# Kernel tuning notes

Hardware: AMD Instinct MI355X
Metric: run time of the kernel (lower is better)

## Reference

```python
import jax, jax.numpy as jnp
import numpy as np

NUM_TOKENS = 4096
HIDDEN = 2048
INTER = 1408
NUM_EXPERTS = 8
TOP_K = 2


def setup_inputs() -> dict:
    key = jax.random.key(0)
    k1, k2, k3, k4, k5 = jax.random.split(key, 5)
    hidden_states = jax.random.normal(k1, (NUM_TOKENS, HIDDEN), dtype=jnp.float32)
    # w1: (E, 2*I, H) gate+up fused; w2: (E, H, I)
    w1 = jax.random.normal(k2, (NUM_EXPERTS, 2 * INTER, HIDDEN), dtype=jnp.float32) * (1.0 / np.sqrt(HIDDEN))
    w2 = jax.random.normal(k3, (NUM_EXPERTS, HIDDEN, INTER), dtype=jnp.float32) * (1.0 / np.sqrt(INTER))
    raw = jax.random.uniform(k4, (NUM_TOKENS, TOP_K), dtype=jnp.float32)
    topk_weights = raw / jnp.sum(raw, axis=-1, keepdims=True)  # router softmax-normalized weights
    topk_ids = jax.random.randint(k5, (NUM_TOKENS, TOP_K), 0, NUM_EXPERTS, dtype=jnp.int32)
    return {"hidden_states": hidden_states, "w1": w1, "w2": w2,
            "topk_weights": topk_weights, "topk_ids": topk_ids}


def reference(hidden_states, w1, w2, topk_weights, topk_ids):
    """Math-equivalent of fused_experts (dispatch -> grouped gate_up GEMM ->
    SwiGLU -> grouped down GEMM -> weighted scatter-combine).

    Expressed densely per expert (E is small and fixed), which yields the
    identical output to the sorted/grouped-GEMM formulation.
    """
    E = w1.shape[0]
    inter = w1.shape[1] // 2
    dtype = hidden_states.dtype
    # gate_up projection for every expert: [E, N, 2I]
    gate_up = jnp.einsum('nh,eih->eni', hidden_states, w1)
    gate, up = gate_up[..., :inter], gate_up[..., inter:]
    act = jax.nn.silu(gate) * up  # npu_swiglu: silu(first half) * second half
    # down projection: [E, N, H]
    expert_out = jnp.einsum('eni,ehi->enh', act, w2)
    # combine weight per (token, expert): sum of topk_weights where routed
    one_hot = jax.nn.one_hot(topk_ids, E, dtype=dtype)          # [N, K, E]
    combine = jnp.sum(topk_weights[:, :, None] * one_hot, axis=1)  # [N, E]
    return jnp.einsum('ne,enh->nh', combine, expert_out)
```

## Files before the change

### kernel.cpp

```cpp
#include <hip/hip_runtime.h>
#include <hip/hip_bf16.h>

#define NTOK 4096
#define HID 2048
#define INTER 1408
#define NEXP 8
#define NPAIR 8192
#define NK1 64
#define NKT2 22
#define G1SZ 24576
#define SZ2 16384

typedef short bf16x8 __attribute__((ext_vector_type(8)));
typedef float f32x4 __attribute__((ext_vector_type(4)));

__device__ __forceinline__ unsigned short f2bf(float f) {
  unsigned u = __builtin_bit_cast(unsigned, f);
  u += 0x7fffu + ((u >> 16) & 1u);
  return (unsigned short)(u >> 16);
}
__device__ __forceinline__ float bf2f(unsigned short v) {
  return __builtin_bit_cast(float, (unsigned)v << 16);
}

__device__ __forceinline__ void gload16(const void* g, void* l) {
  __builtin_amdgcn_global_load_lds(
      (const __attribute__((address_space(1))) void*)g,
      (__attribute__((address_space(3))) void*)l, 16, 0, 0);
}

__device__ __forceinline__ int xcd_swz(int lin, int nwg) {
  int xcd = lin & 7, base = lin >> 3;
  int q = nwg >> 3, r = nwg & 7;
  return (xcd < r ? xcd * (q + 1) : r * (q + 1) + (xcd - r) * q) + base;
}

#define BAR __builtin_amdgcn_s_barrier()
#define SCHED0 __builtin_amdgcn_sched_barrier(0)
#define LGKM0 asm volatile("s_waitcnt lgkmcnt(0)" ::: "memory")
#define VM4 asm volatile("s_waitcnt vmcnt(4)" ::: "memory")
#define VM3 asm volatile("s_waitcnt vmcnt(3)" ::: "memory")
#define VM0 asm volatile("s_waitcnt vmcnt(0)" ::: "memory")
#define PRIO1 __builtin_amdgcn_s_setprio(1)
#define PRIO0 __builtin_amdgcn_s_setprio(0)

__global__ void k_prep(const float* __restrict__ hs, const float* __restrict__ w1,
                       unsigned short* __restrict__ dst,
                       const int* __restrict__ ids, int* __restrict__ ctrl,
                       unsigned short* __restrict__ row_token,
                       unsigned short* __restrict__ inv_row) {
  if (blockIdx.x == 0) {
    __shared__ int cnt[NEXP], cur[NEXP];
    int t = threadIdx.x;
    if (t < NEXP) cnt[t] = 0;
    __syncthreads();
    for (int p = t; p < NPAIR; p += 512) atomicAdd(&cnt[ids[p]], 1);
    __syncthreads();
    if (t == 0) {
      int acc = 0, T = 0;
      for (int e = 0; e < NEXP; ++e) {
        cur[e] = acc;
        ctrl[e] = cnt[e];
        ctrl[8 + e] = acc;
        int n = (cnt[e] + 127) >> 7;
        for (int m = 0; m < n; ++m) { ctrl[32 + T] = e; ctrl[104 + T] = m; ++T; }
        acc += cnt[e];
      }
      ctrl[16] = T;
    }
    __syncthreads();
    for (int p = t; p < NPAIR; p += 512) {
      int e = ids[p];
      int pos = atomicAdd(&cur[e], 1);
      row_token[pos] = (unsigned short)(p >> 1);
      inv_row[p] = (unsigned short)pos;
    }
    return;
  }
  const int N0 = NTOK * HID / 4;
  const int N1 = N0 + NEXP * 2 * INTER * HID / 4;
  int stride = (gridDim.x - 1) * 512;
  for (int i = (blockIdx.x - 1) * 512 + threadIdx.x; i < N1; i += stride) {
    const float* s = (i < N0) ? hs : w1;
    int o = (i < N0) ? i : i - N0;
    float4 v = reinterpret_cast<const float4*>(s)[o];
    ushort4 u;
    u.x = f2bf(v.x); u.y = f2bf(v.y); u.z = f2bf(v.z); u.w = f2bf(v.w);
    reinterpret_cast<ushort4*>(dst)[i] = u;
  }
}


#define G1_STAGE(BB, kt) { \
  gload16(aptr + (size_t)(kt)*32, smem + (BB) + wvb16); \
  gload16(bptr0 + (size_t)(kt)*32, smem + (BB) + 8192 + wvb16); \
  gload16(bptr1 + (size_t)(kt)*32, smem + (BB) + 16384 + wvb16); }

#define G1_RD(BB) { \
  _Pragma("unroll") for (int m_ = 0; m_ < 4; ++m_) \
    af[m_] = *(const bf16x8*)(smem + (BB) + arow + m_*1024 + swz); \
  _Pragma("unroll") for (int n_ = 0; n_ < 2; ++n_) { \
    bg[n_] = *(const bf16x8*)(smem + (BB) + brow + n_*1024 + swz); \
    bu[n_] = *(const bf16x8*)(smem + (BB) + brow + 8192 + n_*1024 + swz); } }

#define G1_MMA \
  _Pragma("unroll") for (int m_ = 0; m_ < 4; ++m_) \
  _Pragma("unroll") for (int n_ = 0; n_ < 2; ++n_) { \
    accg[m_][n_] = __builtin_amdgcn_mfma_f32_16x16x32_bf16(af[m_], bg[n_], accg[m_][n_], 0, 0, 0); \
    accu[m_][n_] = __builtin_amdgcn_mfma_f32_16x16x32_bf16(af[m_], bu[n_], accu[m_][n_], 0, 0, 0); }

__global__ __launch_bounds__(512, 4) void k_gemm1(
    const unsigned short* __restrict__ hs,
    const unsigned short* __restrict__ w1,
    const float* __restrict__ w2f,
    unsigned short* __restrict__ w2b,
    const int* __restrict__ ctrl,
    const unsigned short* __restrict__ row_token,
    unsigned short* __restrict__ act) {
  const int T = ctrl[16];
  const int nwg = T * 11;
  const int lin = blockIdx.x;
  if (lin >= nwg) {
    const int NW2 = NEXP * HID * INTER / 4;
    int nc = gridDim.x - nwg;
    for (int i = (lin - nwg) * 512 + threadIdx.x; i < NW2; i += nc * 512) {
      float4 v = reinterpret_cast<const float4*>(w2f)[i];
      ushort4 u;
      u.x = f2bf(v.x); u.y = f2bf(v.y); u.z = f2bf(v.z); u.w = f2bf(v.w);
      reinterpret_cast<ushort4*>(w2b)[i] = u;
    }
    return;
  }
  const int wg = xcd_swz(lin, nwg);
  const int ti = wg / 11;
  const int nt = wg - ti * 11;
  const int e = ctrl[32 + ti], mt = ctrl[104 + ti];
  const int rows = ctrl[e], off_e = ctrl[8 + e];
  const int n0g = nt * 128;
  const unsigned short* w1e = w1 + (size_t)e * (2 * INTER * HID);

  __shared__ __align__(16) char smem[2 * G1SZ];

  const int t = threadIdx.x;
  const int lane = t & 63, wv = t >> 6;
  const int wm = wv >> 2, wn = wv & 3;
  const int lm = lane & 15, hi4 = lane >> 4;
  const int wvb16 = (t & 448) * 16;
  const int arow = wm * 4096 + lm * 64;
  const int brow = 8192 + wn * 2048 + lm * 64;
  const int swz = (hi4 ^ ((lm >> 1) & 3)) * 16;

  const unsigned short *aptr, *bptr0, *bptr1;
  {
    int cl8 = ((t & 3) ^ ((t >> 3) & 3)) * 8;
    int r = t >> 2;
    int g0 = mt * 128 + r; if (g0 > rows - 1) g0 = rows - 1;
    aptr = hs + (size_t)row_token[off_e + g0] * HID + cl8;
    bptr0 = w1e + (size_t)(n0g + r) * HID + cl8;
    bptr1 = w1e + (size_t)(INTER + n0g + r) * HID + cl8;
  }

  f32x4 accg[4][2], accu[4][2];
#pragma unroll
  for (int m = 0; m < 4; ++m)
#pragma unroll
    for (int n = 0; n < 2; ++n) {
      accg[m][n] = (f32x4){0.f, 0.f, 0.f, 0.f};
      accu[m][n] = (f32x4){0.f, 0.f, 0.f, 0.f};
    }
  bf16x8 af[4], bg[2], bu[2];

  G1_STAGE(0, 0)
  G1_STAGE(G1SZ, 1)
  VM3; BAR;

  unsigned cur = 0, oth = G1SZ;
  for (int kt = 0; kt < NK1; ++kt) {
    G1_RD(cur)
    LGKM0; BAR;
    SCHED0;
    if (kt + 2 < NK1) { G1_STAGE(cur, kt + 2) }
    PRIO1; G1_MMA PRIO0;
    if (kt < NK1 - 2) { VM3; BAR; }
    else if (kt == NK1 - 2) { VM0; BAR; }
    unsigned tmp = cur; cur = oth; oth = tmp;
  }

#pragma unroll
  for (int m = 0; m < 4; ++m)
#pragma unroll
    for (int n = 0; n < 2; ++n) {
      int col = n0g + wn * 32 + n * 16 + lm;
#pragma unroll
      for (int j = 0; j < 4; ++j) {
        int grow = mt * 128 + wm * 64 + m * 16 + hi4 * 4 + j;
        if (grow < rows) {
          float g = accg[m][n][j];
          float u = accu[m][n][j];
          float a = g / (1.0f + __expf(-g)) * u;
          act[(size_t)(off_e + grow) * INTER + col] = f2bf(a);
        }
      }
    }
}

#define G2_RD_A(BB) { \
  _Pragma("unroll") for (int m_ = 0; m_ < 4; ++m_) { \
    af[m_][0] = *(const bf16x8*)(smem + (BB) + aoff + m_*1024 + csw0); \
    af[m_][1] = *(const bf16x8*)(smem + (BB) + aoff + m_*1024 + csw1); } }
#define G2_RD_B(BB) { \
  _Pragma("unroll") for (int n_ = 0; n_ < 2; ++n_) { \
    bfr[n_][0] = *(const bf16x8*)(smem + (BB) + boff + n_*1024 + csw0); \
    bfr[n_][1] = *(const bf16x8*)(smem + (BB) + boff + n_*1024 + csw1); } }

__global__ __launch_bounds__(512, 4) void k_gemm2(
    const unsigned short* __restrict__ act,
    const unsigned short* __restrict__ w2,
    const int* __restrict__ ctrl,
    unsigned short* __restrict__ eo) {
  const int T = ctrl[16];
  const int nwg = T * 16;
  const int lin = blockIdx.x;
  if (lin >= nwg) return;
  const int wg = xcd_swz(lin, nwg);
  const int ti = wg >> 4;
  const int nt = wg & 15;
  const int e = ctrl[32 + ti], mt = ctrl[104 + ti];
  const int rows = ctrl[e], off_e = ctrl[8 + e];
  const int n0 = nt * 128;
  const unsigned short* w2e = w2 + (size_t)e * (HID * INTER);

  __shared__ unsigned short smem[SZ2 * 2];

  const int t = threadIdx.x;
  const int lane = t & 63, wv = t >> 6;
  const int wm = wv >> 2, wn = wv & 3;
  const int lm = lane & 15, hi4 = lane >> 4;
  const int aoff = (wm * 64 + lm) * 64;
  const int boff = 8192 + (wn * 32 + lm) * 64;
  const int csw0 = (hi4 ^ (lm & 7)) * 8;
  const int csw1 = ((4 + hi4) ^ (lm & 7)) * 8;
  const int ldst = t * 8;

  const unsigned short* asrc[2];
#pragma unroll
  for (int i = 0; i < 2; ++i) {
    int p = i * 512 + t;
    int row = p >> 3, c = p & 7;
    int grow = mt * 128 + row;
    if (grow > rows - 1) grow = rows - 1;
    asrc[i] = act + (size_t)(off_e + grow) * INTER + (c ^ (row & 7)) * 8;
  }
  const unsigned short* bsrc[2];
#pragma unroll
  for (int i = 0; i < 2; ++i) {
    int p = i * 512 + t;
    int cb = p >> 3, c = p & 7;
    bsrc[i] = w2e + (size_t)(n0 + cb) * INTER + (c ^ (cb & 7)) * 8;
  }

#define G2_STAGE(BB, kt) { \
  gload16(asrc[0] + (size_t)(kt)*64, smem + (BB) + ldst); \
  gload16(asrc[1] + (size_t)(kt)*64, smem + (BB) + 4096 + ldst); \
  gload16(bsrc[0] + (size_t)(kt)*64, smem + (BB) + 8192 + ldst); \
  gload16(bsrc[1] + (size_t)(kt)*64, smem + (BB) + 12288 + ldst); }

  f32x4 acc[4][2];
#pragma unroll
  for (int m = 0; m < 4; ++m)
#pragma unroll
    for (int n = 0; n < 2; ++n) acc[m][n] = (f32x4){0.f, 0.f, 0.f, 0.f};
  bf16x8 af[4][2], bfr[2][2];

  G2_STAGE(0, 0)
  G2_STAGE(SZ2, 1)
  VM4; BAR;

  unsigned cur = 0, oth = SZ2;
  for (int kt = 0; kt < NKT2; ++kt) {
    G2_RD_A(cur)
    G2_RD_B(cur)
    LGKM0; BAR;
    SCHED0;
    if (kt + 2 < NKT2) { G2_STAGE(cur, kt + 2) }
    PRIO1;
#pragma unroll
    for (int kk = 0; kk < 2; ++kk)
#pragma unroll
      for (int m = 0; m < 4; ++m)
#pragma unroll
        for (int n = 0; n < 2; ++n)
          acc[m][n] = __builtin_amdgcn_mfma_f32_16x16x32_bf16(af[m][kk], bfr[n][kk], acc[m][n], 0, 0, 0);
    PRIO0;
    if (kt < NKT2 - 2) { VM4; BAR; }
    else if (kt == NKT2 - 2) { VM0; BAR; }
    unsigned tmp = cur; cur = oth; oth = tmp;
  }

#pragma unroll
  for (int m = 0; m < 4; ++m)
#pragma unroll
    for (int n = 0; n < 2; ++n) {
      int col = n0 + wn * 32 + n * 16 + lm;
#pragma unroll
      for (int j = 0; j < 4; ++j) {
        int grow = mt * 128 + wm * 64 + m * 16 + hi4 * 4 + j;
        if (grow < rows)
          eo[(size_t)(off_e + grow) * HID + col] = f2bf(acc[m][n][j]);
      }
    }
#undef G2_STAGE
}

__global__ void k_combine(const unsigned short* __restrict__ eo,
                          const float* __restrict__ tw,
                          const unsigned short* __restrict__ inv_row,
                          float* __restrict__ out) {
  int idx = blockIdx.x * blockDim.x + threadIdx.x;
  int tok = idx >> 8;
  int c8 = (idx & 255) * 8;
  int r0 = inv_row[tok * 2], r1 = inv_row[tok * 2 + 1];
  float w0 = tw[tok * 2], w1 = tw[tok * 2 + 1];
  bf16x8 v0 = *(const bf16x8*)(eo + (size_t)r0 * HID + c8);
  bf16x8 v1 = *(const bf16x8*)(eo + (size_t)r1 * HID + c8);
  float4 o0, o1;
  o0.x = w0 * bf2f((unsigned short)v0[0]) + w1 * bf2f((unsigned short)v1[0]);
  o0.y = w0 * bf2f((unsigned short)v0[1]) + w1 * bf2f((unsigned short)v1[1]);
  o0.z = w0 * bf2f((unsigned short)v0[2]) + w1 * bf2f((unsigned short)v1[2]);
  o0.w = w0 * bf2f((unsigned short)v0[3]) + w1 * bf2f((unsigned short)v1[3]);
  o1.x = w0 * bf2f((unsigned short)v0[4]) + w1 * bf2f((unsigned short)v1[4]);
  o1.y = w0 * bf2f((unsigned short)v0[5]) + w1 * bf2f((unsigned short)v1[5]);
  o1.z = w0 * bf2f((unsigned short)v0[6]) + w1 * bf2f((unsigned short)v1[6]);
  o1.w = w0 * bf2f((unsigned short)v0[7]) + w1 * bf2f((unsigned short)v1[7]);
  float4* op = reinterpret_cast<float4*>(out) + (size_t)tok * 512 + (idx & 255) * 2;
  op[0] = o0;
  op[1] = o1;
}

extern "C" void kernel_launch(void* const* d_in, const int* in_sizes, int n_in,
                              void* d_out, int out_size, void* d_ws, size_t ws_size,
                              hipStream_t stream) {
  const float* hs_f = (const float*)d_in[0];
  const float* w1_f = (const float*)d_in[1];
  const float* w2_f = (const float*)d_in[2];
  const float* tw   = (const float*)d_in[3];
  const int*   tids = (const int*)d_in[4];
  float* out = (float*)d_out;

  char* ws = (char*)d_ws;
  unsigned short* hs_b = (unsigned short*)(ws);
  unsigned short* w2_b = (unsigned short*)(ws + 109051904);
  unsigned short* act  = (unsigned short*)(ws + 155189248);
  unsigned short* eo   = (unsigned short*)(ws + 16777216);
  int* ctrl = (int*)(ws + 178257920);
  unsigned short* row_token = (unsigned short*)(ws + 178258944);
  unsigned short* inv_row   = (unsigned short*)(ws + 178275328);

  k_prep<<<2049, 512, 0, stream>>>(hs_f, w1_f, hs_b, tids, ctrl, row_token, inv_row);

  k_gemm1<<<1280, 512, 0, stream>>>(hs_b, (unsigned short*)(ws + 16777216), w2_f, w2_b,
                                    ctrl, row_token, act);
  k_gemm2<<<72 * 16, 512, 0, stream>>>(act, w2_b, ctrl, eo);
  k_combine<<<NTOK * HID / 8 / 256, 256, 0, stream>>>(eo, tw, inv_row, out);
}
```

Measured before the change: 260.7 us.

## Triple-buffer LDS in both expert GEMMs with one barrier per k-step

Both grouped GEMMs move from double to triple LDS buffering. The prefetch for step k+2 now goes into a third buffer right after the fragment reads, so each k-iteration needs only one barrier instead of two. GEMM2 is also reshaped to use K=32 tiles with the same swizzled layout as GEMM1 (44 steps instead of 22), and its launch bound rises to 6 waves per SIMD. The goal is less barrier stall and more latency hiding, at the cost of more LDS per block and more loop iterations in GEMM2.

```diff
diff --git a/kernel.cpp b/kernel.cpp
--- a/kernel.cpp
+++ b/kernel.cpp
@@ -7,9 +7,9 @@
 #define NEXP 8
 #define NPAIR 8192
 #define NK1 64
-#define NKT2 22
+#define NK2 44
 #define G1SZ 24576
-#define SZ2 16384
+#define G2SZ 16384
 
 typedef short bf16x8 __attribute__((ext_vector_type(8)));
 typedef float f32x4 __attribute__((ext_vector_type(4)));
@@ -38,8 +38,8 @@
 #define BAR __builtin_amdgcn_s_barrier()
 #define SCHED0 __builtin_amdgcn_sched_barrier(0)
 #define LGKM0 asm volatile("s_waitcnt lgkmcnt(0)" ::: "memory")
-#define VM4 asm volatile("s_waitcnt vmcnt(4)" ::: "memory")
 #define VM3 asm volatile("s_waitcnt vmcnt(3)" ::: "memory")
+#define VM2 asm volatile("s_waitcnt vmcnt(2)" ::: "memory")
 #define VM0 asm volatile("s_waitcnt vmcnt(0)" ::: "memory")
 #define PRIO1 __builtin_amdgcn_s_setprio(1)
 #define PRIO0 __builtin_amdgcn_s_setprio(0)
@@ -139,7 +139,7 @@
   const int n0g = nt * 128;
   const unsigned short* w1e = w1 + (size_t)e * (2 * INTER * HID);
 
-  __shared__ __align__(16) char smem[2 * G1SZ];
+  __shared__ __align__(16) char smem[3 * G1SZ];
 
   const int t = threadIdx.x;
   const int lane = t & 63, wv = t >> 6;
@@ -170,20 +170,20 @@
     }
   bf16x8 af[4], bg[2], bu[2];
 
-  G1_STAGE(0, 0)
-  G1_STAGE(G1SZ, 1)
+  unsigned bA = 0, bB = G1SZ, bC = 2 * G1SZ;
+  G1_STAGE(bA, 0)
+  G1_STAGE(bB, 1)
   VM3; BAR;
 
-  unsigned cur = 0, oth = G1SZ;
   for (int kt = 0; kt < NK1; ++kt) {
-    G1_RD(cur)
+    G1_RD(bA)
+    if (kt + 2 < NK1) { G1_STAGE(bC, kt + 2) }
+    SCHED0;
+    PRIO1; G1_MMA PRIO0;
+    if (kt < NK1 - 2) { VM3; }
+    else if (kt == NK1 - 2) { VM0; }
     LGKM0; BAR;
-    SCHED0;
-    if (kt + 2 < NK1) { G1_STAGE(cur, kt + 2) }
-    PRIO1; G1_MMA PRIO0;
-    if (kt < NK1 - 2) { VM3; BAR; }
-    else if (kt == NK1 - 2) { VM0; BAR; }
-    unsigned tmp = cur; cur = oth; oth = tmp;
+    unsigned tmp = bA; bA = bB; bB = bC; bC = tmp;
   }
 
 #pragma unroll
@@ -204,16 +204,22 @@
     }
 }
 
-#define G2_RD_A(BB) { \
-  _Pragma("unroll") for (int m_ = 0; m_ < 4; ++m_) { \
-    af[m_][0] = *(const bf16x8*)(smem + (BB) + aoff + m_*1024 + csw0); \
-    af[m_][1] = *(const bf16x8*)(smem + (BB) + aoff + m_*1024 + csw1); } }
-#define G2_RD_B(BB) { \
-  _Pragma("unroll") for (int n_ = 0; n_ < 2; ++n_) { \
-    bfr[n_][0] = *(const bf16x8*)(smem + (BB) + boff + n_*1024 + csw0); \
-    bfr[n_][1] = *(const bf16x8*)(smem + (BB) + boff + n_*1024 + csw1); } }
-
-__global__ __launch_bounds__(512, 4) void k_gemm2(
+#define G2_STAGE(BB, kt) { \
+  gload16(aptr + (size_t)(kt)*32, smem + (BB) + wvb16); \
+  gload16(bptr + (size_t)(kt)*32, smem + (BB) + 8192 + wvb16); }
+
+#define G2_RD(BB) { \
+  _Pragma("unroll") for (int m_ = 0; m_ < 4; ++m_) \
+    af[m_] = *(const bf16x8*)(smem + (BB) + arow + m_*1024 + swz); \
+  _Pragma("unroll") for (int n_ = 0; n_ < 2; ++n_) \
+    bn[n_] = *(const bf16x8*)(smem + (BB) + brow + n_*1024 + swz); }
+
+#define G2_MMA \
+  _Pragma("unroll") for (int m_ = 0; m_ < 4; ++m_) \
+  _Pragma("unroll") for (int n_ = 0; n_ < 2; ++n_) \
+    acc[m_][n_] = __builtin_amdgcn_mfma_f32_16x16x32_bf16(af[m_], bn[n_], acc[m_][n_], 0, 0, 0);
+
+__global__ __launch_bounds__(512, 6) void k_gemm2(
     const unsigned short* __restrict__ act,
     const unsigned short* __restrict__ w2,
     const int* __restrict__ ctrl,
@@ -230,71 +236,47 @@
   const int n0 = nt * 128;
   const unsigned short* w2e = w2 + (size_t)e * (HID * INTER);
 
-  __shared__ unsigned short smem[SZ2 * 2];
+  __shared__ __align__(16) char smem[3 * G2SZ];
 
   const int t = threadIdx.x;
   const int lane = t & 63, wv = t >> 6;
   const int wm = wv >> 2, wn = wv & 3;
   const int lm = lane & 15, hi4 = lane >> 4;
-  const int aoff = (wm * 64 + lm) * 64;
-  const int boff = 8192 + (wn * 32 + lm) * 64;
-  const int csw0 = (hi4 ^ (lm & 7)) * 8;
-  const int csw1 = ((4 + hi4) ^ (lm & 7)) * 8;
-  const int ldst = t * 8;
-
-  const unsigned short* asrc[2];
-#pragma unroll
-  for (int i = 0; i < 2; ++i) {
-    int p = i * 512 + t;
-    int row = p >> 3, c = p & 7;
-    int grow = mt * 128 + row;
-    if (grow > rows - 1) grow = rows - 1;
-    asrc[i] = act + (size_t)(off_e + grow) * INTER + (c ^ (row & 7)) * 8;
-  }
-  const unsigned short* bsrc[2];
-#pragma unroll
-  for (int i = 0; i < 2; ++i) {
-    int p = i * 512 + t;
-    int cb = p >> 3, c = p & 7;
-    bsrc[i] = w2e + (size_t)(n0 + cb) * INTER + (c ^ (cb & 7)) * 8;
-  }
-
-#define G2_STAGE(BB, kt) { \
-  gload16(asrc[0] + (size_t)(kt)*64, smem + (BB) + ldst); \
-  gload16(asrc[1] + (size_t)(kt)*64, smem + (BB) + 4096 + ldst); \
-  gload16(bsrc[0] + (size_t)(kt)*64, smem + (BB) + 8192 + ldst); \
-  gload16(bsrc[1] + (size_t)(kt)*64, smem + (BB) + 12288 + ldst); }
+  const int wvb16 = (t & 448) * 16;
+  const int arow = wm * 4096 + lm * 64;
+  const int brow = 8192 + wn * 2048 + lm * 64;
+  const int swz = (hi4 ^ ((lm >> 1) & 3)) * 16;
+
+  const unsigned short *aptr, *bptr;
+  {
+    int cl8 = ((t & 3) ^ ((t >> 3) & 3)) * 8;
+    int r = t >> 2;
+    int g0 = mt * 128 + r; if (g0 > rows - 1) g0 = rows - 1;
+    aptr = act + (size_t)(off_e + g0) * INTER + cl8;
+    bptr = w2e + (size_t)(n0 + r) * INTER + cl8;
+  }
 
   f32x4 acc[4][2];
 #pragma unroll
   for (int m = 0; m < 4; ++m)
 #pragma unroll
     for (int n = 0; n < 2; ++n) acc[m][n] = (f32x4){0.f, 0.f, 0.f, 0.f};
-  bf16x8 af[4][2], bfr[2][2];
-
-  G2_STAGE(0, 0)
-  G2_STAGE(SZ2, 1)
-  VM4; BAR;
-
-  unsigned cur = 0, oth = SZ2;
-  for (int kt = 0; kt < NKT2; ++kt) {
-    G2_RD_A(cur)
-    G2_RD_B(cur)
+  bf16x8 af[4], bn[2];
+
+  unsigned bA = 0, bB = G2SZ, bC = 2 * G2SZ;
+  G2_STAGE(bA, 0)
+  G2_STAGE(bB, 1)
+  VM2; BAR;
+
+  for (int kt = 0; kt < NK2; ++kt) {
+    G2_RD(bA)
+    if (kt + 2 < NK2) { G2_STAGE(bC, kt + 2) }
+    SCHED0;
+    PRIO1; G2_MMA PRIO0;
+    if (kt < NK2 - 2) { VM2; }
+    else if (kt == NK2 - 2) { VM0; }
     LGKM0; BAR;
-    SCHED0;
-    if (kt + 2 < NKT2) { G2_STAGE(cur, kt + 2) }
-    PRIO1;
-#pragma unroll
-    for (int kk = 0; kk < 2; ++kk)
-#pragma unroll
-      for (int m = 0; m < 4; ++m)
-#pragma unroll
-        for (int n = 0; n < 2; ++n)
-          acc[m][n] = __builtin_amdgcn_mfma_f32_16x16x32_bf16(af[m][kk], bfr[n][kk], acc[m][n], 0, 0, 0);
-    PRIO0;
-    if (kt < NKT2 - 2) { VM4; BAR; }
-    else if (kt == NKT2 - 2) { VM0; BAR; }
-    unsigned tmp = cur; cur = oth; oth = tmp;
+    unsigned tmp = bA; bA = bB; bB = bC; bC = tmp;
   }
 
 #pragma unroll
@@ -309,7 +291,6 @@
           eo[(size_t)(off_e + grow) * HID + col] = f2bf(acc[m][n][j]);
       }
     }
-#undef G2_STAGE
 }
 
 __global__ void k_combine(const unsigned short* __restrict__ eo,
```

Result: no change. 263.0 us (+0.9%).
